# Optimization experiments

Hardware: AMD Instinct MI355X
Metric: run time of the kernel (lower is better)

## Reference

```python
import jax, jax.numpy as jnp
import numpy as np

NUM_CLASSES = 256
SIGMA = 5.0
BATCH = 262144


def setup_inputs() -> dict:
    key = jax.random.key(0)
    k1, k2 = jax.random.split(key)
    logits = jax.random.normal(k1, (BATCH, NUM_CLASSES), dtype=jnp.float32)
    targets = jax.random.randint(k2, (BATCH,), 0, NUM_CLASSES, dtype=jnp.int64)
    return {"logits": logits, "targets": targets}


def reference(logits, targets):
    # Soft targets: quartic-exponent Gaussian-like kernel around true class, normalized.
    # distances[b, c] = c - targets[b]
    classes = jnp.arange(NUM_CLASSES, dtype=jnp.float32)  # (C,)
    d = classes[None, :] - targets[:, None].astype(jnp.float32)  # (B, C)
    w = jnp.exp(-(d ** 4) / (2.0 * SIGMA ** 2))  # (B, C)
    soft = w / jnp.sum(w, axis=1, keepdims=True)

    log_probs = jax.nn.log_softmax(logits, axis=1)  # (B, C)

    # KLDivLoss(reduction='batchmean'): sum(t * (log t - log p)) / batch,
    # with the convention 0 * log 0 = 0.
    t_log_t = jnp.where(soft > 0, soft * jnp.log(jnp.where(soft > 0, soft, 1.0)), 0.0)
    loss = jnp.sum(t_log_t - soft * log_probs) / logits.shape[0]
    return loss
```

## Files before the change

kernel.cpp:

```cpp
#include <hip/hip_runtime.h>

#define NCLS 256

#define DPP_ADD(x, ctrl) \
    ((x) + __int_as_float(__builtin_amdgcn_update_dpp( \
        0, __float_as_int(x), (ctrl), 0xF, 0xF, true)))

__device__ __forceinline__ float red16(float x) {
    x = DPP_ADD(x, 0xB1);
    x = DPP_ADD(x, 0x4E);
    x = DPP_ADD(x, 0x141);
    x = DPP_ADD(x, 0x140);
    return x;
}

__global__ __launch_bounds__(256) void SmoothOrdinalLoss_kernel(
    const float* __restrict__ logits,
    const int* __restrict__ targets,
    float* __restrict__ out,
    int batch)
{
    __shared__ float  wtab[512];
    __shared__ float2 ab[NCLS];
    __shared__ float  part[4];

    const int tid = threadIdx.x;

    wtab[tid]       = 0.0f;
    wtab[tid + 256] = 0.0f;
    if (tid < 17) {
        float d  = (float)(tid - 8);
        float d2 = d * d;
        wtab[tid] = __expf(-(d2 * d2) * 0.02f);
    }
    {
        const int t = tid;
        float sw = 0.0f, swlw = 0.0f;
        #pragma unroll
        for (int d = -8; d <= 8; ++d) {
            int c = t + d;
            if (c >= 0 && c < NCLS) {
                float fd = (float)d;
                float a  = (fd * fd) * (fd * fd) * 0.02f;
                float w  = __expf(-a);
                sw += w;
                swlw = fmaf(w, -a, swlw);
            }
        }
        float invS = 1.0f / sw;
        ab[t] = make_float2(fmaf(swlw, invS, -__logf(sw)), invS);
    }
    __syncthreads();

    const int lane = tid & 63;
    const int wib  = tid >> 6;
    const int g    = lane >> 4;
    const int li   = lane & 15;

    const int wave    = blockIdx.x * 4 + wib;
    const int nwaves  = gridDim.x * 4;
    const int nchunks = batch >> 2;

    float acc = 0.0f;

    for (int ch = wave; ch < nchunks; ch += nwaves) {
        const int row = ch * 4 + g;
        const float4* rp =
            reinterpret_cast<const float4*>(logits + (size_t)row * NCLS);
        float4 v0 = rp[li];
        float4 v1 = rp[li + 16];
        float4 v2 = rp[li + 32];
        float4 v3 = rp[li + 48];
        const int t      = targets[row];
        const int duBase = li * 4 + 8 - t;

        float xs[16] = {v0.x, v0.y, v0.z, v0.w,  v1.x, v1.y, v1.z, v1.w,
                        v2.x, v2.y, v2.z, v2.w,  v3.x, v3.y, v3.z, v3.w};

        float z = 0.0f, swx = 0.0f;
        #pragma unroll
        for (int k = 0; k < 4; ++k) {
            #pragma unroll
            for (int j = 0; j < 4; ++j) {
                float x = xs[k * 4 + j];
                z += __expf(x);
                int idx = (duBase + k * 64 + j) & 511;
                swx = fmaf(wtab[idx], x, swx);
            }
        }

        z   = red16(z);
        swx = red16(swx);

        float2 c = ab[t];
        acc += c.x - swx * c.y + __logf(z);
    }

    acc += __shfl_xor(acc, 16);
    acc += __shfl_xor(acc, 32);
    if (lane == 0) part[wib] = acc;
    __syncthreads();
    if (tid == 0) {
        float s = (part[0] + part[1] + part[2] + part[3]) / (float)batch;
        atomicAdd(out, s);
    }
}

extern "C" void kernel_launch(void* const* d_in, const int* in_sizes, int n_in,
                              void* d_out, int out_size, void* d_ws, size_t ws_size,
                              hipStream_t stream) {
    const float* logits  = (const float*)d_in[0];
    const int*   targets = (const int*)d_in[1];
    float*       out     = (float*)d_out;
    const int batch = in_sizes[1];

    hipMemsetAsync(d_out, 0, sizeof(float), stream);

    dim3 block(256);
    dim3 grid(2048);
    SmoothOrdinalLoss_kernel<<<grid, block, 0, stream>>>(logits, targets, out, batch);
}
```

Before: 57.51 us.

## Double-buffer row loads, use nontemporal loads, compute soft weights inline

Software-pipelines the grid-stride loop by issuing the next chunk's loads into a second register set before computing the current one, so memory latency overlaps compute. Loads switch to nontemporal hints to avoid polluting cache with streamed logits. The shared-memory weight table is removed: each lane picks the one float4 that can contain the ±8 window and evaluates the weights with exp directly, replacing 16 LDS reads per row with 4 exps. This costs more registers, which may lower occupancy.

```diff
diff --git a/kernel.cpp b/kernel.cpp
--- a/kernel.cpp
+++ b/kernel.cpp
@@ -1,6 +1,8 @@
 #include <hip/hip_runtime.h>
 
 #define NCLS 256
+
+typedef float f32x4_t __attribute__((ext_vector_type(4)));
 
 #define DPP_ADD(x, ctrl) \
     ((x) + __int_as_float(__builtin_amdgcn_update_dpp( \
@@ -20,19 +22,11 @@
     float* __restrict__ out,
     int batch)
 {
-    __shared__ float  wtab[512];
     __shared__ float2 ab[NCLS];
     __shared__ float  part[4];
 
     const int tid = threadIdx.x;
 
-    wtab[tid]       = 0.0f;
-    wtab[tid + 256] = 0.0f;
-    if (tid < 17) {
-        float d  = (float)(tid - 8);
-        float d2 = d * d;
-        wtab[tid] = __expf(-(d2 * d2) * 0.02f);
-    }
     {
         const int t = tid;
         float sw = 0.0f, swlw = 0.0f;
@@ -63,37 +57,65 @@
 
     float acc = 0.0f;
 
-    for (int ch = wave; ch < nchunks; ch += nwaves) {
+    auto loadch = [&](int ch, f32x4_t& v0, f32x4_t& v1, f32x4_t& v2,
+                      f32x4_t& v3, int& t) {
         const int row = ch * 4 + g;
-        const float4* rp =
-            reinterpret_cast<const float4*>(logits + (size_t)row * NCLS);
-        float4 v0 = rp[li];
-        float4 v1 = rp[li + 16];
-        float4 v2 = rp[li + 32];
-        float4 v3 = rp[li + 48];
-        const int t      = targets[row];
-        const int duBase = li * 4 + 8 - t;
+        const f32x4_t* rp =
+            reinterpret_cast<const f32x4_t*>(logits + (size_t)row * NCLS);
+        v0 = __builtin_nontemporal_load(rp + li);
+        v1 = __builtin_nontemporal_load(rp + li + 16);
+        v2 = __builtin_nontemporal_load(rp + li + 32);
+        v3 = __builtin_nontemporal_load(rp + li + 48);
+        t  = targets[row];
+    };
 
-        float xs[16] = {v0.x, v0.y, v0.z, v0.w,  v1.x, v1.y, v1.z, v1.w,
-                        v2.x, v2.y, v2.z, v2.w,  v3.x, v3.y, v3.z, v3.w};
+    auto compute = [&](f32x4_t v0, f32x4_t v1, f32x4_t v2, f32x4_t v3, int t) {
+        float z0 = (__expf(v0.x) + __expf(v0.y)) + (__expf(v0.z) + __expf(v0.w));
+        float z1 = (__expf(v1.x) + __expf(v1.y)) + (__expf(v1.z) + __expf(v1.w));
+        float z2 = (__expf(v2.x) + __expf(v2.y)) + (__expf(v2.z) + __expf(v2.w));
+        float z3 = (__expf(v3.x) + __expf(v3.y)) + (__expf(v3.z) + __expf(v3.w));
+        float z  = (z0 + z1) + (z2 + z3);
 
-        float z = 0.0f, swx = 0.0f;
+        int u  = t - 4 * li;
+        int ks = (u + 32) >> 6;
+        ks = ks < 0 ? 0 : (ks > 3 ? 3 : ks);
+        f32x4_t xs = (ks < 2) ? (ks == 0 ? v0 : v1) : (ks == 2 ? v2 : v3);
+
+        float base = (float)(4 * li + 64 * ks - t);
+        float sw = 0.0f;
         #pragma unroll
-        for (int k = 0; k < 4; ++k) {
-            #pragma unroll
-            for (int j = 0; j < 4; ++j) {
-                float x = xs[k * 4 + j];
-                z += __expf(x);
-                int idx = (duBase + k * 64 + j) & 511;
-                swx = fmaf(wtab[idx], x, swx);
-            }
+        for (int j = 0; j < 4; ++j) {
+            float d  = base + (float)j;
+            float d2 = d * d;
+            float a  = d2 * d2 * 0.02f;
+            float w  = __expf(-a);
+            sw = fmaf(w, xs[j], sw);
         }
 
-        z   = red16(z);
-        swx = red16(swx);
+        z  = red16(z);
+        sw = red16(sw);
 
         float2 c = ab[t];
-        acc += c.x - swx * c.y + __logf(z);
+        acc += c.x - sw * c.y + __logf(z);
+    };
+
+    f32x4_t a0, a1, a2, a3, b0, b1, b2, b3;
+    int ta, tb;
+
+    int ch = wave;
+    bool havA = ch < nchunks;
+    if (havA) loadch(ch, a0, a1, a2, a3, ta);
+    while (havA) {
+        int chB = ch + nwaves;
+        bool havB = chB < nchunks;
+        if (havB) loadch(chB, b0, b1, b2, b3, tb);
+        compute(a0, a1, a2, a3, ta);
+        if (!havB) break;
+        int chA = chB + nwaves;
+        havA = chA < nchunks;
+        if (havA) loadch(chA, a0, a1, a2, a3, ta);
+        compute(b0, b1, b2, b3, tb);
+        ch = chA;
     }
 
     acc += __shfl_xor(acc, 16);
```

Result: slower. 59.40 us (+3.3%).

## Map one wave per row with contiguous loads and compute weights in-register

Applied to the files above, without the earlier changes.

Each wave now processes four rows one at a time, with all 64 lanes loading a contiguous float4 slice of the same row, instead of 16-lane groups each handling a different row. The shared-memory weight table is dropped and the quartic Gaussian weights are recomputed per element with an extra exp, which removes LDS lookups and bank conflicts. Every lane adds the per-row constant and the log partition term, so these are scaled by 1/64 at the end while the weighted term is reduced across the wave after the loop. In exchange each row needs a full 64-lane reduction with cross-row shuffles, and each element needs roughly twice as many transcendental operations.

```diff
diff --git a/kernel.cpp b/kernel.cpp
--- a/kernel.cpp
+++ b/kernel.cpp
@@ -1,6 +1,8 @@
 #include <hip/hip_runtime.h>
 
 #define NCLS 256
+
+typedef float f32x4_t __attribute__((ext_vector_type(4)));
 
 #define DPP_ADD(x, ctrl) \
     ((x) + __int_as_float(__builtin_amdgcn_update_dpp( \
@@ -14,25 +16,24 @@
     return x;
 }
 
+__device__ __forceinline__ float red64(float x) {
+    x = red16(x);
+    x += __shfl_xor(x, 16);
+    x += __shfl_xor(x, 32);
+    return x;
+}
+
 __global__ __launch_bounds__(256) void SmoothOrdinalLoss_kernel(
     const float* __restrict__ logits,
     const int* __restrict__ targets,
     float* __restrict__ out,
     int batch)
 {
-    __shared__ float  wtab[512];
     __shared__ float2 ab[NCLS];
     __shared__ float  part[4];
 
     const int tid = threadIdx.x;
 
-    wtab[tid]       = 0.0f;
-    wtab[tid + 256] = 0.0f;
-    if (tid < 17) {
-        float d  = (float)(tid - 8);
-        float d2 = d * d;
-        wtab[tid] = __expf(-(d2 * d2) * 0.02f);
-    }
     {
         const int t = tid;
         float sw = 0.0f, swlw = 0.0f;
@@ -54,50 +55,53 @@
 
     const int lane = tid & 63;
     const int wib  = tid >> 6;
-    const int g    = lane >> 4;
-    const int li   = lane & 15;
 
     const int wave    = blockIdx.x * 4 + wib;
     const int nwaves  = gridDim.x * 4;
     const int nchunks = batch >> 2;
 
-    float acc = 0.0f;
+    float accW = 0.0f;
+    float accU = 0.0f;
+
+    const float fl4 = (float)(4 * lane);
 
     for (int ch = wave; ch < nchunks; ch += nwaves) {
-        const int row = ch * 4 + g;
-        const float4* rp =
-            reinterpret_cast<const float4*>(logits + (size_t)row * NCLS);
-        float4 v0 = rp[li];
-        float4 v1 = rp[li + 16];
-        float4 v2 = rp[li + 32];
-        float4 v3 = rp[li + 48];
-        const int t      = targets[row];
-        const int duBase = li * 4 + 8 - t;
+        const int rbase = ch * 4;
+        const float* bp = logits + (size_t)rbase * NCLS;
+        f32x4_t v0 = reinterpret_cast<const f32x4_t*>(bp)[lane];
+        f32x4_t v1 = reinterpret_cast<const f32x4_t*>(bp + NCLS)[lane];
+        f32x4_t v2 = reinterpret_cast<const f32x4_t*>(bp + 2 * NCLS)[lane];
+        f32x4_t v3 = reinterpret_cast<const f32x4_t*>(bp + 3 * NCLS)[lane];
 
-        float xs[16] = {v0.x, v0.y, v0.z, v0.w,  v1.x, v1.y, v1.z, v1.w,
-                        v2.x, v2.y, v2.z, v2.w,  v3.x, v3.y, v3.z, v3.w};
-
-        float z = 0.0f, swx = 0.0f;
-        #pragma unroll
-        for (int k = 0; k < 4; ++k) {
-            #pragma unroll
-            for (int j = 0; j < 4; ++j) {
-                float x = xs[k * 4 + j];
-                z += __expf(x);
-                int idx = (duBase + k * 64 + j) & 511;
-                swx = fmaf(wtab[idx], x, swx);
-            }
+        #define ROW(vk, k)                                                  \
+        {                                                                   \
+            const int t = targets[rbase + (k)];           \
+            const float2 c = ab[t];                                         \
+            float zp = (__expf(vk.x) + __expf(vk.y))                        \
+                     + (__expf(vk.z) + __expf(vk.w));                       \
+            float z = red64(zp);                                            \
+            accU += c.x + __logf(z);                                        \
+            float db = fl4 - (float)t;                                      \
+            float swxl = 0.0f;                                              \
+            _Pragma("unroll")                                               \
+            for (int j = 0; j < 4; ++j) {                                   \
+                float d  = db + (float)j;                                   \
+                float d2 = d * d;                                           \
+                float a  = d2 * d2 * 0.02f;   \
+                swxl = fmaf(__expf(-a), vk[j], swxl);                       \
+            }                                                               \
+            accW = fmaf(-c.y, swxl, accW);                                  \
         }
 
-        z   = red16(z);
-        swx = red16(swx);
-
-        float2 c = ab[t];
-        acc += c.x - swx * c.y + __logf(z);
+        ROW(v0, 0)
+        ROW(v1, 1)
+        ROW(v2, 2)
+        ROW(v3, 3)
+        #undef ROW
     }
 
-    acc += __shfl_xor(acc, 16);
-    acc += __shfl_xor(acc, 32);
+    float acc = fmaf(accU, 1.0f / 64.0f, accW);
+    acc = red64(acc);
     if (lane == 0) part[wib] = acc;
     __syncthreads();
     if (tid == 0) {
```

Result: slower. 61.46 us (+6.9%).

## Defer weighted-sum reduction to kernel end and replace atomic with two-pass reduce

Applied to the files above, without the earlier changes.

Moves the per-row cross-lane reduction of the weighted logit sum out of the loop: each lane accumulates its partial sum times the row's inverse weight sum, and the whole thing is reduced once at the end. The per-row constant terms are scaled by 1/16 to make up for being added on all 16 lanes. The weight table is laid out with an offset so indexing needs no masking. The memset and atomicAdd are replaced by per-block partials in the workspace plus a one-block reduce kernel, which costs an extra launch but removes the memset and the atomic contention.

```diff
diff --git a/kernel.cpp b/kernel.cpp
--- a/kernel.cpp
+++ b/kernel.cpp
@@ -1,6 +1,8 @@
 #include <hip/hip_runtime.h>
 
 #define NCLS 256
+
+typedef float f32x4_t __attribute__((ext_vector_type(4)));
 
 #define DPP_ADD(x, ctrl) \
     ((x) + __int_as_float(__builtin_amdgcn_update_dpp( \
@@ -14,10 +16,17 @@
     return x;
 }
 
-__global__ __launch_bounds__(256) void SmoothOrdinalLoss_kernel(
+__device__ __forceinline__ float red64(float x) {
+    x = red16(x);
+    x += __shfl_xor(x, 16);
+    x += __shfl_xor(x, 32);
+    return x;
+}
+
+__global__ __launch_bounds__(256) void SmoothOrdinalLoss_main(
     const float* __restrict__ logits,
     const int* __restrict__ targets,
-    float* __restrict__ out,
+    float* __restrict__ ws,
     int batch)
 {
     __shared__ float  wtab[512];
@@ -26,14 +35,18 @@
 
     const int tid = threadIdx.x;
 
-    wtab[tid]       = 0.0f;
-    wtab[tid + 256] = 0.0f;
-    if (tid < 17) {
-        float d  = (float)(tid - 8);
-        float d2 = d * d;
-        wtab[tid] = __expf(-(d2 * d2) * 0.02f);
-    }
     {
+        #pragma unroll
+        for (int h = 0; h < 2; ++h) {
+            int idx = tid + 256 * h;
+            int d   = idx - 256;
+            float w = 0.0f;
+            if (d >= -8 && d <= 8) {
+                float fd = (float)d;
+                w = __expf(-(fd * fd) * (fd * fd) * 0.02f);
+            }
+            wtab[idx] = w;
+        }
         const int t = tid;
         float sw = 0.0f, swlw = 0.0f;
         #pragma unroll
@@ -61,49 +74,65 @@
     const int nwaves  = gridDim.x * 4;
     const int nchunks = batch >> 2;
 
-    float acc = 0.0f;
+    float accU = 0.0f;
+    float accW = 0.0f;
+
+    const int li4 = li * 4;
 
     for (int ch = wave; ch < nchunks; ch += nwaves) {
         const int row = ch * 4 + g;
-        const float4* rp =
-            reinterpret_cast<const float4*>(logits + (size_t)row * NCLS);
-        float4 v0 = rp[li];
-        float4 v1 = rp[li + 16];
-        float4 v2 = rp[li + 32];
-        float4 v3 = rp[li + 48];
-        const int t      = targets[row];
-        const int duBase = li * 4 + 8 - t;
+        const f32x4_t* rp =
+            reinterpret_cast<const f32x4_t*>(logits + (size_t)row * NCLS);
+        f32x4_t v0 = rp[li];
+        f32x4_t v1 = rp[li + 16];
+        f32x4_t v2 = rp[li + 32];
+        f32x4_t v3 = rp[li + 48];
+        const int t = targets[row];
 
+        float z0 = (__expf(v0.x) + __expf(v0.y)) + (__expf(v0.z) + __expf(v0.w));
+        float z1 = (__expf(v1.x) + __expf(v1.y)) + (__expf(v1.z) + __expf(v1.w));
+        float z2 = (__expf(v2.x) + __expf(v2.y)) + (__expf(v2.z) + __expf(v2.w));
+        float z3 = (__expf(v3.x) + __expf(v3.y)) + (__expf(v3.z) + __expf(v3.w));
+        float z  = red16((z0 + z1) + (z2 + z3));
+
+        const float* wp = &wtab[li4 + 256 - t];
         float xs[16] = {v0.x, v0.y, v0.z, v0.w,  v1.x, v1.y, v1.z, v1.w,
                         v2.x, v2.y, v2.z, v2.w,  v3.x, v3.y, v3.z, v3.w};
-
-        float z = 0.0f, swx = 0.0f;
+        float swxl = 0.0f;
         #pragma unroll
         for (int k = 0; k < 4; ++k) {
             #pragma unroll
-            for (int j = 0; j < 4; ++j) {
-                float x = xs[k * 4 + j];
-                z += __expf(x);
-                int idx = (duBase + k * 64 + j) & 511;
-                swx = fmaf(wtab[idx], x, swx);
-            }
+            for (int j = 0; j < 4; ++j)
+                swxl = fmaf(wp[64 * k + j], xs[k * 4 + j], swxl);
         }
 
-        z   = red16(z);
-        swx = red16(swx);
-
         float2 c = ab[t];
-        acc += c.x - swx * c.y + __logf(z);
+        accU += c.x + __logf(z);
+        accW  = fmaf(swxl, c.y, accW);
     }
 
-    acc += __shfl_xor(acc, 16);
-    acc += __shfl_xor(acc, 32);
+    float acc = red64(fmaf(accU, 0.0625f, -accW));
     if (lane == 0) part[wib] = acc;
     __syncthreads();
-    if (tid == 0) {
-        float s = (part[0] + part[1] + part[2] + part[3]) / (float)batch;
-        atomicAdd(out, s);
-    }
+    if (tid == 0)
+        ws[blockIdx.x] = (part[0] + part[1]) + (part[2] + part[3]);
+}
+
+__global__ __launch_bounds__(256) void SmoothOrdinalLoss_reduce(
+    const float* __restrict__ ws,
+    float* __restrict__ out,
+    int nparts, float invB)
+{
+    __shared__ float part[4];
+    const int tid = threadIdx.x;
+    float s = 0.0f;
+    for (int i = tid; i < nparts; i += 256) s += ws[i];
+    s = red64(s);
+    const int lane = tid & 63, wib = tid >> 6;
+    if (lane == 0) part[wib] = s;
+    __syncthreads();
+    if (tid == 0)
+        out[0] = ((part[0] + part[1]) + (part[2] + part[3])) * invB;
 }
 
 extern "C" void kernel_launch(void* const* d_in, const int* in_sizes, int n_in,
@@ -112,11 +141,12 @@
     const float* logits  = (const float*)d_in[0];
     const int*   targets = (const int*)d_in[1];
     float*       out     = (float*)d_out;
+    float*       ws      = (float*)d_ws;
     const int batch = in_sizes[1];
 
-    hipMemsetAsync(d_out, 0, sizeof(float), stream);
-
-    dim3 block(256);
-    dim3 grid(2048);
-    SmoothOrdinalLoss_kernel<<<grid, block, 0, stream>>>(logits, targets, out, batch);
+    const int nblocks = 2048;
+    SmoothOrdinalLoss_main<<<dim3(nblocks), dim3(256), 0, stream>>>(
+        logits, targets, ws, batch);
+    SmoothOrdinalLoss_reduce<<<dim3(1), dim3(256), 0, stream>>>(
+        ws, out, nblocks, 1.0f / (float)batch);
 }
```

New measurement: 46.68 us. 18.8% less time.
